# Kernel tuning notes

Hardware: AMD Instinct MI355X
Metric: run time of the kernel (lower is better)

The kernel has to match this reference:

```python
import math
import jax, jax.numpy as jnp
import numpy as np

D_MODEL = 2048
NUM_HEADS = 16

def setup_inputs() -> dict:
    key = jax.random.key(0)
    k1, k2, k3, k4, k5 = jax.random.split(key, 5)
    s = 1.0 / math.sqrt(D_MODEL)
    return {
        "in_features": jax.random.normal(k1, (2, 2048, D_MODEL), dtype=jnp.float32),
        "q_proj": jax.random.normal(k2, (D_MODEL, D_MODEL), dtype=jnp.float32) * s,
        "k_proj": jax.random.normal(k3, (D_MODEL, D_MODEL), dtype=jnp.float32) * s,
        "v_proj": jax.random.normal(k4, (D_MODEL, D_MODEL), dtype=jnp.float32) * s,
        "o_proj": jax.random.normal(k5, (D_MODEL, D_MODEL), dtype=jnp.float32) * s,
    }

def reference(in_features, q_proj, k_proj, v_proj, o_proj):
    B, S, D = in_features.shape
    H = NUM_HEADS
    d_k = D // H
    # x @ W.T, then split heads: [B, H, S, d_k]
    def proj(W):
        return (in_features @ W.T).reshape(B, S, H, d_k).transpose(0, 2, 1, 3)
    Q, K, V = proj(q_proj), proj(k_proj), proj(v_proj)
    scores = jnp.einsum("bhqd,bhkd->bhqk", Q, K) / math.sqrt(d_k)
    causal = jnp.triu(jnp.ones((S, S), dtype=bool), k=1)  # True above diagonal
    scores = jnp.where(causal, -jnp.inf, scores)
    attn = jax.nn.softmax(scores, axis=-1)
    out = jnp.einsum("bhqk,bhkd->bhqd", attn, V)
    out = out.transpose(0, 2, 1, 3).reshape(B, S, D)
    return out @ o_proj.T
```

## Files before the change

### kernel.cpp

```cpp
#include <hip/hip_runtime.h>
#include <math.h>
#include <stdint.h>

#define D_MODEL 2048
#define NHEAD   16
#define DK      128
#define SEQ     2048
#define BATCH   2
#define MROWS   (BATCH * SEQ)

typedef __bf16 bf16;
typedef __bf16 bf16x8 __attribute__((ext_vector_type(8)));
typedef __bf16 bf16x4 __attribute__((ext_vector_type(4)));
typedef float  f32x4  __attribute__((ext_vector_type(4)));

__device__ __forceinline__ bf16 f2bf(float f) {
    unsigned u = __builtin_bit_cast(unsigned, f);
    u += 0x7fffu + ((u >> 16) & 1u);
    unsigned short h = (unsigned short)(u >> 16);
    return __builtin_bit_cast(bf16, h);
}

#define GLDS16(gp, lp)                                                        \
    __builtin_amdgcn_global_load_lds(                                         \
        (__attribute__((address_space(1))) void*)(uintptr_t)(gp),             \
        (__attribute__((address_space(3))) void*)(lp), 16, 0, 0)

#define QSCALE 0.08838834764831845f

__global__ void cvt_f32_bf16(const float* __restrict__ src,
                             bf16* __restrict__ dst, int n4) {
    int i = blockIdx.x * blockDim.x + threadIdx.x;
    if (i < n4) {
        float4 v = ((const float4*)src)[i];
        bf16x4 o;
        o[0] = f2bf(v.x); o[1] = f2bf(v.y); o[2] = f2bf(v.z); o[3] = f2bf(v.w);
        *(bf16x4*)(dst + (size_t)i * 4) = o;
    }
}

__global__ __launch_bounds__(256)
void gemm_qkv(const bf16* __restrict__ A, const bf16* __restrict__ B,
              bf16* __restrict__ Qb, bf16* __restrict__ Kbf,
              bf16* __restrict__ Vt) {
    __shared__ alignas(16) bf16 sA[128 * 32];
    __shared__ alignas(16) bf16 sB[128 * 32];
    const int K = D_MODEL;

    const int tid  = threadIdx.x;
    const int lane = tid & 63;
    const int wid  = tid >> 6;
    const int wm   = wid >> 1, wn = wid & 1;
    const int brow = blockIdx.y * 128, bcol = blockIdx.x * 128;
    const int r16  = lane & 15, g = lane >> 4;

    f32x4 acc[4][4] = {};

    const int c0 = tid, c1 = 256 + tid;
    const int rowS0 = c0 >> 2, colS0 = (c0 & 3) * 8;
    const int rowS1 = c1 >> 2, colS1 = (c1 & 3) * 8;

    for (int kt = 0; kt < K; kt += 32) {
        GLDS16(A + (size_t)(brow + rowS0) * K + kt + colS0, &sA[c0 * 8]);
        GLDS16(A + (size_t)(brow + rowS1) * K + kt + colS1, &sA[c1 * 8]);
        GLDS16(B + (size_t)(bcol + rowS0) * K + kt + colS0, &sB[c0 * 8]);
        GLDS16(B + (size_t)(bcol + rowS1) * K + kt + colS1, &sB[c1 * 8]);
        __syncthreads();

        bf16x8 af[4], bfr[4];
#pragma unroll
        for (int m = 0; m < 4; ++m)
            af[m] = *(const bf16x8*)&sA[(wm * 64 + m * 16 + r16) * 32 + g * 8];
#pragma unroll
        for (int n = 0; n < 4; ++n)
            bfr[n] = *(const bf16x8*)&sB[(wn * 64 + n * 16 + r16) * 32 + g * 8];
#pragma unroll
        for (int m = 0; m < 4; ++m)
#pragma unroll
            for (int n = 0; n < 4; ++n)
                acc[m][n] = __builtin_amdgcn_mfma_f32_16x16x32_bf16(
                    af[m], bfr[n], acc[m][n], 0, 0, 0);
        __syncthreads();
    }

    const int which = bcol >> 11;
#pragma unroll
    for (int m = 0; m < 4; ++m) {
#pragma unroll
        for (int n = 0; n < 4; ++n) {
            const int col  = bcol + wn * 64 + n * 16 + r16;
            const int row0 = brow + wm * 64 + m * 16 + g * 4;
            if (which == 0) {
#pragma unroll
                for (int r = 0; r < 4; ++r)
                    Qb[(size_t)(row0 + r) * D_MODEL + col] =
                        f2bf(acc[m][n][r] * QSCALE);
            } else if (which == 1) {
#pragma unroll
                for (int r = 0; r < 4; ++r)
                    Kbf[(size_t)(row0 + r) * D_MODEL + (col - 2048)] =
                        f2bf(acc[m][n][r]);
            } else {
                const int b = row0 >> 11, s = row0 & 2047;
                bf16x4 v;
#pragma unroll
                for (int r = 0; r < 4; ++r) v[r] = f2bf(acc[m][n][r]);
                *(bf16x4*)&Vt[(size_t)(b * 2048 + (col - 4096)) * 2048 + s] = v;
            }
        }
    }
}

__global__ __launch_bounds__(256)
void gemm_o(const bf16* __restrict__ A, const bf16* __restrict__ B,
            float* __restrict__ C) {
    __shared__ alignas(16) bf16 sA[128 * 32];
    __shared__ alignas(16) bf16 sB[128 * 32];
    const int K = D_MODEL, N = D_MODEL;

    const int tid  = threadIdx.x;
    const int lane = tid & 63;
    const int wid  = tid >> 6;
    const int wm   = wid >> 1, wn = wid & 1;
    const int brow = blockIdx.y * 128, bcol = blockIdx.x * 128;
    const int r16  = lane & 15, g = lane >> 4;

    f32x4 acc[4][4] = {};

    const int c0 = tid, c1 = 256 + tid;
    const int rowS0 = c0 >> 2, colS0 = (c0 & 3) * 8;
    const int rowS1 = c1 >> 2, colS1 = (c1 & 3) * 8;

    for (int kt = 0; kt < K; kt += 32) {
        GLDS16(A + (size_t)(brow + rowS0) * K + kt + colS0, &sA[c0 * 8]);
        GLDS16(A + (size_t)(brow + rowS1) * K + kt + colS1, &sA[c1 * 8]);
        GLDS16(B + (size_t)(bcol + rowS0) * K + kt + colS0, &sB[c0 * 8]);
        GLDS16(B + (size_t)(bcol + rowS1) * K + kt + colS1, &sB[c1 * 8]);
        __syncthreads();

        bf16x8 af[4], bfr[4];
#pragma unroll
        for (int m = 0; m < 4; ++m)
            af[m] = *(const bf16x8*)&sA[(wm * 64 + m * 16 + r16) * 32 + g * 8];
#pragma unroll
        for (int n = 0; n < 4; ++n)
            bfr[n] = *(const bf16x8*)&sB[(wn * 64 + n * 16 + r16) * 32 + g * 8];
#pragma unroll
        for (int m = 0; m < 4; ++m)
#pragma unroll
            for (int n = 0; n < 4; ++n)
                acc[m][n] = __builtin_amdgcn_mfma_f32_16x16x32_bf16(
                    af[m], bfr[n], acc[m][n], 0, 0, 0);
        __syncthreads();
    }

#pragma unroll
    for (int m = 0; m < 4; ++m)
#pragma unroll
        for (int n = 0; n < 4; ++n) {
            const int col  = bcol + wn * 64 + n * 16 + r16;
            const int row0 = brow + wm * 64 + m * 16 + g * 4;
#pragma unroll
            for (int r = 0; r < 4; ++r)
                C[(size_t)(row0 + r) * N + col] = acc[m][n][r];
        }
}

__global__ __launch_bounds__(256, 2)
void attn_fwd(const bf16* __restrict__ Q, const bf16* __restrict__ Kb,
              const bf16* __restrict__ Vt, bf16* __restrict__ AO) {
    __shared__ alignas(16) bf16 sK[2][64 * 128];
    __shared__ alignas(16) bf16 P_lds[4][32][72];

    const int tid  = threadIdx.x;
    const int lane = tid & 63;
    const int wid  = tid >> 6;
    const int r16  = lane & 15, g = lane >> 4;
    const int bh   = blockIdx.y;
    const int b    = bh >> 4;
    const int qt   = (blockIdx.y & 16) ? (15 - (int)blockIdx.x)
                                       : (int)blockIdx.x;
    const int qbase = qt * 128 + wid * 32;
    const size_t rowbase = (size_t)b * SEQ;
    const int hcol = (bh & 15) * DK;
    const int nt   = 2 * qt + 2;

    bf16x8 aq[2][4];
#pragma unroll
    for (int m = 0; m < 2; ++m) {
        const bf16* qp =
            Q + (rowbase + qbase + m * 16 + r16) * D_MODEL + hcol + g * 8;
#pragma unroll
        for (int c = 0; c < 4; ++c) aq[m][c] = *(const bf16x8*)(qp + c * 32);
    }

    f32x4 o[2][8] = {};
    float m_run[2][4], l_run[2][4];
#pragma unroll
    for (int m = 0; m < 2; ++m)
#pragma unroll
        for (int r = 0; r < 4; ++r) {
            m_run[m][r] = -3.0e38f;
            l_run[m][r] = 0.f;
        }

    auto stage = [&](int buf, int t) {
        const int kv0 = t * 64;
#pragma unroll
        for (int j = 0; j < 4; ++j) {
            const int ldsOff = wid * 1024 + j * 4096 + lane * 16;
            const int row    = ldsOff >> 8;
            const int colB   = (lane & 15) * 16;
            const int scolB  = colB ^ ((row & 7) << 4);
            const bf16* gp =
                Kb + (rowbase + kv0 + row) * D_MODEL + hcol + (scolB >> 1);
            GLDS16(gp, (bf16*)sK[buf] + (ldsOff >> 1));
        }
    };

    int cur = 0;
    stage(0, 0);
    __syncthreads();

    for (int t = 0; t < nt; ++t) {
        if (t + 1 < nt) stage(cur ^ 1, t + 1);
        const int kv0 = t * 64;

        if (kv0 <= qbase + 31) {
            f32x4 s[2][4] = {};
#pragma unroll
            for (int c = 0; c < 4; ++c) {
                bf16x8 kf[4];
#pragma unroll
                for (int n = 0; n < 4; ++n) {
                    const int row  = n * 16 + r16;
                    const int colB = (c * 64 + g * 16) ^ ((row & 7) << 4);
                    kf[n] = *(const bf16x8*)&sK[cur][row * 128 + (colB >> 1)];
                }
#pragma unroll
                for (int n = 0; n < 4; ++n)
#pragma unroll
                    for (int m = 0; m < 2; ++m)
                        s[m][n] = __builtin_amdgcn_mfma_f32_16x16x32_bf16(
                            aq[m][c], kf[n], s[m][n], 0, 0, 0);
            }

            if (kv0 + 63 > qbase) {
#pragma unroll
                for (int m = 0; m < 2; ++m)
#pragma unroll
                    for (int n = 0; n < 4; ++n)
#pragma unroll
                        for (int r = 0; r < 4; ++r) {
                            int kvg = kv0 + n * 16 + r16;
                            int qg  = qbase + m * 16 + g * 4 + r;
                            if (kvg > qg) s[m][n][r] = -3.0e38f;
                        }
            }

            float tm[2][4];
#pragma unroll
            for (int m = 0; m < 2; ++m)
#pragma unroll
                for (int r = 0; r < 4; ++r)
                    tm[m][r] = fmaxf(fmaxf(s[m][0][r], s[m][1][r]),
                                     fmaxf(s[m][2][r], s[m][3][r]));
#pragma unroll
            for (int d = 1; d < 16; d <<= 1)
#pragma unroll
                for (int m = 0; m < 2; ++m)
#pragma unroll
                    for (int r = 0; r < 4; ++r)
                        tm[m][r] = fmaxf(tm[m][r], __shfl_xor(tm[m][r], d));

            float alpha[2][4];
#pragma unroll
            for (int m = 0; m < 2; ++m)
#pragma unroll
                for (int r = 0; r < 4; ++r) {
                    float nm    = fmaxf(m_run[m][r], tm[m][r]);
                    alpha[m][r] = __expf(m_run[m][r] - nm);
                    m_run[m][r] = nm;
                }
#pragma unroll
            for (int m = 0; m < 2; ++m)
#pragma unroll
                for (int n = 0; n < 4; ++n)
#pragma unroll
                    for (int r = 0; r < 4; ++r)
                        s[m][n][r] = __expf(s[m][n][r] - m_run[m][r]);

            float rs[2][4];
#pragma unroll
            for (int m = 0; m < 2; ++m)
#pragma unroll
                for (int r = 0; r < 4; ++r)
                    rs[m][r] = (s[m][0][r] + s[m][1][r]) +
                               (s[m][2][r] + s[m][3][r]);
#pragma unroll
            for (int d = 1; d < 16; d <<= 1)
#pragma unroll
                for (int m = 0; m < 2; ++m)
#pragma unroll
                    for (int r = 0; r < 4; ++r)
                        rs[m][r] += __shfl_xor(rs[m][r], d);
#pragma unroll
            for (int m = 0; m < 2; ++m)
#pragma unroll
                for (int r = 0; r < 4; ++r)
                    l_run[m][r] = l_run[m][r] * alpha[m][r] + rs[m][r];
#pragma unroll
            for (int m = 0; m < 2; ++m)
#pragma unroll
                for (int dt = 0; dt < 8; ++dt)
#pragma unroll
                    for (int r = 0; r < 4; ++r) o[m][dt][r] *= alpha[m][r];

#pragma unroll
            for (int m = 0; m < 2; ++m)
#pragma unroll
                for (int n = 0; n < 4; ++n)
#pragma unroll
                    for (int r = 0; r < 4; ++r)
                        P_lds[wid][m * 16 + g * 4 + r][n * 16 + r16] =
                            f2bf(s[m][n][r]);

            bf16x8 pa[2][2];
#pragma unroll
            for (int m = 0; m < 2; ++m)
#pragma unroll
                for (int c = 0; c < 2; ++c)
                    pa[m][c] = *(const bf16x8*)&P_lds[wid][m * 16 + r16]
                                                    [c * 32 + g * 8];

            const bf16* vp = Vt + ((size_t)bh * DK) * SEQ + kv0 + g * 8;
#pragma unroll
            for (int dt = 0; dt < 8; ++dt) {
                bf16x8 bv[2];
#pragma unroll
                for (int c = 0; c < 2; ++c)
                    bv[c] = *(const bf16x8*)(vp +
                                             (size_t)(dt * 16 + r16) * SEQ +
                                             c * 32);
#pragma unroll
                for (int m = 0; m < 2; ++m)
#pragma unroll
                    for (int c = 0; c < 2; ++c)
                        o[m][dt] = __builtin_amdgcn_mfma_f32_16x16x32_bf16(
                            pa[m][c], bv[c], o[m][dt], 0, 0, 0);
            }
        }

        __syncthreads();
        cur ^= 1;
    }

#pragma unroll
    for (int m = 0; m < 2; ++m) {
        float rl[4];
#pragma unroll
        for (int r = 0; r < 4; ++r) rl[r] = 1.f / l_run[m][r];
#pragma unroll
        for (int dt = 0; dt < 8; ++dt)
#pragma unroll
            for (int r = 0; r < 4; ++r) {
                float val = o[m][dt][r] * rl[r];
                AO[(rowbase + qbase + m * 16 + g * 4 + r) * D_MODEL + hcol +
                   dt * 16 + r16] = f2bf(val);
            }
    }
}

extern "C" void kernel_launch(void* const* d_in, const int* in_sizes, int n_in,
                              void* d_out, int out_size, void* d_ws,
                              size_t ws_size, hipStream_t stream) {
    const float* X  = (const float*)d_in[0];
    const float* Wq = (const float*)d_in[1];
    const float* Wk = (const float*)d_in[2];
    const float* Wv = (const float*)d_in[3];
    const float* Wo = (const float*)d_in[4];

    bf16* base = (bf16*)d_ws;
    const size_t NX = (size_t)MROWS * D_MODEL;
    const size_t NW = (size_t)D_MODEL * D_MODEL;
    bf16* Xb  = base;
    bf16* Qb  = Xb + NX;
    bf16* Kbf = Qb + NX;
    bf16* Vt  = Kbf + NX;
    bf16* AOb = Vt + NX;
    bf16* Wqb = AOb + NX;
    bf16* Wkb = Wqb + NW;
    bf16* Wvb = Wkb + NW;
    bf16* Wob = Wvb + NW;

    cvt_f32_bf16<<<(int)(NX / 4 / 256), 256, 0, stream>>>(X, Xb, (int)(NX / 4));
    cvt_f32_bf16<<<(int)(NW / 4 / 256), 256, 0, stream>>>(Wq, Wqb, (int)(NW / 4));
    cvt_f32_bf16<<<(int)(NW / 4 / 256), 256, 0, stream>>>(Wk, Wkb, (int)(NW / 4));
    cvt_f32_bf16<<<(int)(NW / 4 / 256), 256, 0, stream>>>(Wv, Wvb, (int)(NW / 4));
    cvt_f32_bf16<<<(int)(NW / 4 / 256), 256, 0, stream>>>(Wo, Wob, (int)(NW / 4));

    gemm_qkv<<<dim3(48, 32), 256, 0, stream>>>(Xb, Wqb, Qb, Kbf, Vt);

    attn_fwd<<<dim3(SEQ / 128, BATCH * NHEAD), 256, 0, stream>>>(Qb, Kbf, Vt,
                                                                 AOb);

    gemm_o<<<dim3(16, 32), 256, 0, stream>>>(AOb, Wob, (float*)d_out);
}
```

Measured before the change: 531.9 us.

## Fuse conversion kernels, drop LDS K staging, remap attention block order

Merges the five fp32-to-bf16 conversion launches into one grid-stride kernel. In attention, drops the double-buffered LDS staging of K and the block barriers; each wave now reads K fragments straight from global memory and loops only over its own causal tiles. Blocks are remapped so consecutive blocks share a query tile across heads, and the occupancy hint is removed. This trades shared K reuse across the four waves for less synchronisation and fewer wasted iterations, so global/L2 traffic for K goes up.

Result: no change. 541.0 us (+1.7%).

```diff
diff --git a/kernel.cpp b/kernel.cpp
--- a/kernel.cpp
+++ b/kernel.cpp
@@ -28,14 +28,32 @@
 
 #define QSCALE 0.08838834764831845f
 
-__global__ void cvt_f32_bf16(const float* __restrict__ src,
-                             bf16* __restrict__ dst, int n4) {
-    int i = blockIdx.x * blockDim.x + threadIdx.x;
-    if (i < n4) {
-        float4 v = ((const float4*)src)[i];
+__global__ void cvt_all(const float* __restrict__ X, const float* __restrict__ W0,
+                        const float* __restrict__ W1, const float* __restrict__ W2,
+                        const float* __restrict__ W3, bf16* __restrict__ dX,
+                        bf16* __restrict__ dW) {
+    const int NX4 = (MROWS * D_MODEL) / 4;
+    const int NW4 = (D_MODEL * D_MODEL) / 4;
+    const int TOT = NX4 + 4 * NW4;
+    const int stride = gridDim.x * blockDim.x;
+    for (int i = blockIdx.x * blockDim.x + threadIdx.x; i < TOT; i += stride) {
+        const float* sp;
+        bf16* dp;
+        if (i < NX4) {
+            sp = X + (size_t)i * 4;
+            dp = dX + (size_t)i * 4;
+        } else {
+            int j = i - NX4;
+            int s = j >> 20;
+            int off = j & (NW4 - 1);
+            const float* w = (s == 0) ? W0 : (s == 1) ? W1 : (s == 2) ? W2 : W3;
+            sp = w + (size_t)off * 4;
+            dp = dW + ((size_t)s << 22) + (size_t)off * 4;
+        }
+        float4 v = *(const float4*)sp;
         bf16x4 o;
         o[0] = f2bf(v.x); o[1] = f2bf(v.y); o[2] = f2bf(v.z); o[3] = f2bf(v.w);
-        *(bf16x4*)(dst + (size_t)i * 4) = o;
+        *(bf16x4*)dp = o;
     }
 }
 
@@ -166,24 +184,22 @@
         }
 }
 
-__global__ __launch_bounds__(256, 2)
+__global__ __launch_bounds__(256)
 void attn_fwd(const bf16* __restrict__ Q, const bf16* __restrict__ Kb,
               const bf16* __restrict__ Vt, bf16* __restrict__ AO) {
-    __shared__ alignas(16) bf16 sK[2][64 * 128];
     __shared__ alignas(16) bf16 P_lds[4][32][72];
 
     const int tid  = threadIdx.x;
     const int lane = tid & 63;
     const int wid  = tid >> 6;
     const int r16  = lane & 15, g = lane >> 4;
-    const int bh   = blockIdx.y;
+    const int lin  = (int)blockIdx.x + 16 * (int)blockIdx.y;
+    const int bh   = (lin & 7) * 4 + ((lin >> 3) & 3);
+    const int qt   = lin >> 5;
     const int b    = bh >> 4;
-    const int qt   = (blockIdx.y & 16) ? (15 - (int)blockIdx.x)
-                                       : (int)blockIdx.x;
     const int qbase = qt * 128 + wid * 32;
     const size_t rowbase = (size_t)b * SEQ;
     const int hcol = (bh & 15) * DK;
-    const int nt   = 2 * qt + 2;
 
     bf16x8 aq[2][4];
 #pragma unroll
@@ -204,155 +220,129 @@
             l_run[m][r] = 0.f;
         }
 
-    auto stage = [&](int buf, int t) {
+    const int ntile = (qbase >> 6) + 1;
+    for (int t = 0; t < ntile; ++t) {
         const int kv0 = t * 64;
-#pragma unroll
-        for (int j = 0; j < 4; ++j) {
-            const int ldsOff = wid * 1024 + j * 4096 + lane * 16;
-            const int row    = ldsOff >> 8;
-            const int colB   = (lane & 15) * 16;
-            const int scolB  = colB ^ ((row & 7) << 4);
-            const bf16* gp =
-                Kb + (rowbase + kv0 + row) * D_MODEL + hcol + (scolB >> 1);
-            GLDS16(gp, (bf16*)sK[buf] + (ldsOff >> 1));
-        }
-    };
-
-    int cur = 0;
-    stage(0, 0);
-    __syncthreads();
-
-    for (int t = 0; t < nt; ++t) {
-        if (t + 1 < nt) stage(cur ^ 1, t + 1);
-        const int kv0 = t * 64;
-
-        if (kv0 <= qbase + 31) {
-            f32x4 s[2][4] = {};
-#pragma unroll
-            for (int c = 0; c < 4; ++c) {
-                bf16x8 kf[4];
-#pragma unroll
-                for (int n = 0; n < 4; ++n) {
-                    const int row  = n * 16 + r16;
-                    const int colB = (c * 64 + g * 16) ^ ((row & 7) << 4);
-                    kf[n] = *(const bf16x8*)&sK[cur][row * 128 + (colB >> 1)];
-                }
+
+        f32x4 s[2][4] = {};
+#pragma unroll
+        for (int c = 0; c < 4; ++c) {
+            bf16x8 kf[4];
+#pragma unroll
+            for (int n = 0; n < 4; ++n)
+                kf[n] = *(const bf16x8*)(Kb +
+                                         (rowbase + kv0 + n * 16 + r16) *
+                                             D_MODEL +
+                                         hcol + c * 32 + g * 8);
+#pragma unroll
+            for (int n = 0; n < 4; ++n)
+#pragma unroll
+                for (int m = 0; m < 2; ++m)
+                    s[m][n] = __builtin_amdgcn_mfma_f32_16x16x32_bf16(
+                        aq[m][c], kf[n], s[m][n], 0, 0, 0);
+        }
+
+        if (kv0 + 63 > qbase) {
+#pragma unroll
+            for (int m = 0; m < 2; ++m)
 #pragma unroll
                 for (int n = 0; n < 4; ++n)
 #pragma unroll
-                    for (int m = 0; m < 2; ++m)
-                        s[m][n] = __builtin_amdgcn_mfma_f32_16x16x32_bf16(
-                            aq[m][c], kf[n], s[m][n], 0, 0, 0);
+                    for (int r = 0; r < 4; ++r) {
+                        int kvg = kv0 + n * 16 + r16;
+                        int qg  = qbase + m * 16 + g * 4 + r;
+                        if (kvg > qg) s[m][n][r] = -3.0e38f;
+                    }
+        }
+
+        float tm[2][4];
+#pragma unroll
+        for (int m = 0; m < 2; ++m)
+#pragma unroll
+            for (int r = 0; r < 4; ++r)
+                tm[m][r] = fmaxf(fmaxf(s[m][0][r], s[m][1][r]),
+                                 fmaxf(s[m][2][r], s[m][3][r]));
+#pragma unroll
+        for (int d = 1; d < 16; d <<= 1)
+#pragma unroll
+            for (int m = 0; m < 2; ++m)
+#pragma unroll
+                for (int r = 0; r < 4; ++r)
+                    tm[m][r] = fmaxf(tm[m][r], __shfl_xor(tm[m][r], d));
+
+        float alpha[2][4];
+#pragma unroll
+        for (int m = 0; m < 2; ++m)
+#pragma unroll
+            for (int r = 0; r < 4; ++r) {
+                float nm    = fmaxf(m_run[m][r], tm[m][r]);
+                alpha[m][r] = __expf(m_run[m][r] - nm);
+                m_run[m][r] = nm;
             }
-
-            if (kv0 + 63 > qbase) {
-#pragma unroll
-                for (int m = 0; m < 2; ++m)
-#pragma unroll
-                    for (int n = 0; n < 4; ++n)
-#pragma unroll
-                        for (int r = 0; r < 4; ++r) {
-                            int kvg = kv0 + n * 16 + r16;
-                            int qg  = qbase + m * 16 + g * 4 + r;
-                            if (kvg > qg) s[m][n][r] = -3.0e38f;
-                        }
-            }
-
-            float tm[2][4];
+#pragma unroll
+        for (int m = 0; m < 2; ++m)
+#pragma unroll
+            for (int n = 0; n < 4; ++n)
+#pragma unroll
+                for (int r = 0; r < 4; ++r)
+                    s[m][n][r] = __expf(s[m][n][r] - m_run[m][r]);
+
+        float rs[2][4];
+#pragma unroll
+        for (int m = 0; m < 2; ++m)
+#pragma unroll
+            for (int r = 0; r < 4; ++r)
+                rs[m][r] = (s[m][0][r] + s[m][1][r]) + (s[m][2][r] + s[m][3][r]);
+#pragma unroll
+        for (int d = 1; d < 16; d <<= 1)
 #pragma unroll
             for (int m = 0; m < 2; ++m)
 #pragma unroll
-                for (int r = 0; r < 4; ++r)
-                    tm[m][r] = fmaxf(fmaxf(s[m][0][r], s[m][1][r]),
-                                     fmaxf(s[m][2][r], s[m][3][r]));
-#pragma unroll
-            for (int d = 1; d < 16; d <<= 1)
-#pragma unroll
-                for (int m = 0; m < 2; ++m)
-#pragma unroll
-                    for (int r = 0; r < 4; ++r)
-                        tm[m][r] = fmaxf(tm[m][r], __shfl_xor(tm[m][r], d));
-
-            float alpha[2][4];
+                for (int r = 0; r < 4; ++r) rs[m][r] += __shfl_xor(rs[m][r], d);
+#pragma unroll
+        for (int m = 0; m < 2; ++m)
+#pragma unroll
+            for (int r = 0; r < 4; ++r)
+                l_run[m][r] = l_run[m][r] * alpha[m][r] + rs[m][r];
+#pragma unroll
+        for (int m = 0; m < 2; ++m)
+#pragma unroll
+            for (int dt = 0; dt < 8; ++dt)
+#pragma unroll
+                for (int r = 0; r < 4; ++r) o[m][dt][r] *= alpha[m][r];
+
+#pragma unroll
+        for (int m = 0; m < 2; ++m)
+#pragma unroll
+            for (int n = 0; n < 4; ++n)
+#pragma unroll
+                for (int r = 0; r < 4; ++r)
+                    P_lds[wid][m * 16 + g * 4 + r][n * 16 + r16] =
+                        f2bf(s[m][n][r]);
+
+        bf16x8 pa[2][2];
+#pragma unroll
+        for (int m = 0; m < 2; ++m)
+#pragma unroll
+            for (int c = 0; c < 2; ++c)
+                pa[m][c] =
+                    *(const bf16x8*)&P_lds[wid][m * 16 + r16][c * 32 + g * 8];
+
+        const bf16* vp = Vt + ((size_t)bh * DK) * SEQ + kv0 + g * 8;
+#pragma unroll
+        for (int dt = 0; dt < 8; ++dt) {
+            bf16x8 bv[2];
+#pragma unroll
+            for (int c = 0; c < 2; ++c)
+                bv[c] = *(const bf16x8*)(vp + (size_t)(dt * 16 + r16) * SEQ +
+                                         c * 32);
 #pragma unroll
             for (int m = 0; m < 2; ++m)
 #pragma unroll
-                for (int r = 0; r < 4; ++r) {
-                    float nm    = fmaxf(m_run[m][r], tm[m][r]);
-                    alpha[m][r] = __expf(m_run[m][r] - nm);
-                    m_run[m][r] = nm;
-                }
-#pragma unroll
-            for (int m = 0; m < 2; ++m)
-#pragma unroll
-                for (int n = 0; n < 4; ++n)
-#pragma unroll
-                    for (int r = 0; r < 4; ++r)
-                        s[m][n][r] = __expf(s[m][n][r] - m_run[m][r]);
-
-            float rs[2][4];
-#pragma unroll
-            for (int m = 0; m < 2; ++m)
-#pragma unroll
-                for (int r = 0; r < 4; ++r)
-                    rs[m][r] = (s[m][0][r] + s[m][1][r]) +
-                               (s[m][2][r] + s[m][3][r]);
-#pragma unroll
-            for (int d = 1; d < 16; d <<= 1)
-#pragma unroll
-                for (int m = 0; m < 2; ++m)
-#pragma unroll
-                    for (int r = 0; r < 4; ++r)
-                        rs[m][r] += __shfl_xor(rs[m][r], d);
-#pragma unroll
-            for (int m = 0; m < 2; ++m)
-#pragma unroll
-                for (int r = 0; r < 4; ++r)
-                    l_run[m][r] = l_run[m][r] * alpha[m][r] + rs[m][r];
-#pragma unroll
-            for (int m = 0; m < 2; ++m)
-#pragma unroll
-                for (int dt = 0; dt < 8; ++dt)
-#pragma unroll
-                    for (int r = 0; r < 4; ++r) o[m][dt][r] *= alpha[m][r];
-
-#pragma unroll
-            for (int m = 0; m < 2; ++m)
-#pragma unroll
-                for (int n = 0; n < 4; ++n)
-#pragma unroll
-                    for (int r = 0; r < 4; ++r)
-                        P_lds[wid][m * 16 + g * 4 + r][n * 16 + r16] =
-                            f2bf(s[m][n][r]);
-
-            bf16x8 pa[2][2];
-#pragma unroll
-            for (int m = 0; m < 2; ++m)
-#pragma unroll
                 for (int c = 0; c < 2; ++c)
-                    pa[m][c] = *(const bf16x8*)&P_lds[wid][m * 16 + r16]
-                                                    [c * 32 + g * 8];
-
-            const bf16* vp = Vt + ((size_t)bh * DK) * SEQ + kv0 + g * 8;
-#pragma unroll
-            for (int dt = 0; dt < 8; ++dt) {
-                bf16x8 bv[2];
-#pragma unroll
-                for (int c = 0; c < 2; ++c)
-                    bv[c] = *(const bf16x8*)(vp +
-                                             (size_t)(dt * 16 + r16) * SEQ +
-                                             c * 32);
-#pragma unroll
-                for (int m = 0; m < 2; ++m)
-#pragma unroll
-                    for (int c = 0; c < 2; ++c)
-                        o[m][dt] = __builtin_amdgcn_mfma_f32_16x16x32_bf16(
-                            pa[m][c], bv[c], o[m][dt], 0, 0, 0);
-            }
-        }
-
-        __syncthreads();
-        cur ^= 1;
+                    o[m][dt] = __builtin_amdgcn_mfma_f32_16x16x32_bf16(
+                        pa[m][c], bv[c], o[m][dt], 0, 0, 0);
+        }
     }
 
 #pragma unroll
@@ -392,17 +382,13 @@
     bf16* Wkb = Wqb + NW;
     bf16* Wvb = Wkb + NW;
     bf16* Wob = Wvb + NW;
-
-    cvt_f32_bf16<<<(int)(NX / 4 / 256), 256, 0, stream>>>(X, Xb, (int)(NX / 4));
-    cvt_f32_bf16<<<(int)(NW / 4 / 256), 256, 0, stream>>>(Wq, Wqb, (int)(NW / 4));
-    cvt_f32_bf16<<<(int)(NW / 4 / 256), 256, 0, stream>>>(Wk, Wkb, (int)(NW / 4));
-    cvt_f32_bf16<<<(int)(NW / 4 / 256), 256, 0, stream>>>(Wv, Wvb, (int)(NW / 4));
-    cvt_f32_bf16<<<(int)(NW / 4 / 256), 256, 0, stream>>>(Wo, Wob, (int)(NW / 4));
+    (void)Wkb; (void)Wvb;
+
+    cvt_all<<<2048, 256, 0, stream>>>(X, Wq, Wk, Wv, Wo, Xb, Wqb);
 
     gemm_qkv<<<dim3(48, 32), 256, 0, stream>>>(Xb, Wqb, Qb, Kbf, Vt);
 
-    attn_fwd<<<dim3(SEQ / 128, BATCH * NHEAD), 256, 0, stream>>>(Qb, Kbf, Vt,
-                                                                 AOb);
+    attn_fwd<<<dim3(16, 32), 256, 0, stream>>>(Qb, Kbf, Vt, AOb);
 
     gemm_o<<<dim3(16, 32), 256, 0, stream>>>(AOb, Wob, (float*)d_out);
 }
```
